# Performance work log

Hardware: AMD Instinct MI355X
Metric: run time of the kernel (lower is better)

Reference implementation:

```python
import jax, jax.numpy as jnp
import numpy as np

TOP_K = 30
NUM_RBF = 16
MAX_REL = 32  # max_relative_feature
LN_EPS = 1e-5


def normalize(x, axis=-1, eps=1e-12):
    n = jnp.linalg.norm(x, axis=axis, keepdims=True)
    return x / jnp.maximum(n, eps)


def gather_nodes(nodes, idx):
    # nodes [B,L,C], idx [B,L,K] -> [B,L,K,C]
    B, L, K = idx.shape
    flat = idx.reshape(B, L * K)
    g = jnp.take_along_axis(nodes, flat[:, :, None], axis=1)
    return g.reshape(B, L, K, -1)


def gather_edges(edges, idx):
    # edges [B,L,L,C], idx [B,L,K] -> [B,L,K,C]
    return jnp.take_along_axis(edges, idx[..., None], axis=2)


def _dist(Xca, mask, eps=1e-6):
    mask_2D = mask[:, None, :] * mask[:, :, None]            # [B,L,L]
    dX = Xca[:, None, :, :] - Xca[:, :, None, :]             # [B,L,L,3]
    D = mask_2D * jnp.sqrt(jnp.sum(dX ** 2, -1) + eps)
    D_max = jnp.max(D, -1, keepdims=True)
    D_adjust = D + (1.0 - mask_2D) * D_max
    k = min(TOP_K, Xca.shape[1])
    neg_vals, E_idx = jax.lax.top_k(-D_adjust, k)            # smallest-k
    D_neighbors = -neg_vals
    mask_neighbors = gather_edges(mask_2D[..., None], E_idx)
    return D_neighbors, E_idx, mask_neighbors


def _rbf(D):
    D_mu = jnp.linspace(2.0, 22.0, NUM_RBF)                  # [R]
    D_sigma = (22.0 - 2.0) / NUM_RBF
    return jnp.exp(-(((D[..., None] - D_mu) / D_sigma) ** 2))


def _quaternions(R):
    # R [...,3,3] -> Q [...,4]
    diag = jnp.diagonal(R, axis1=-2, axis2=-1)               # [...,3]
    Rxx, Ryy, Rzz = diag[..., 0], diag[..., 1], diag[..., 2]
    mags = 0.5 * jnp.sqrt(jnp.abs(1 + jnp.stack(
        [Rxx - Ryy - Rzz, -Rxx + Ryy - Rzz, -Rxx - Ryy + Rzz], -1)))
    signs = jnp.sign(jnp.stack([
        R[..., 2, 1] - R[..., 1, 2],
        R[..., 0, 2] - R[..., 2, 0],
        R[..., 1, 0] - R[..., 0, 1]], -1))
    xyz = signs * mags
    w = jnp.sqrt(jax.nn.relu(1 + jnp.sum(diag, -1, keepdims=True))) / 2.0
    return normalize(jnp.concatenate([xyz, w], -1))


def _get_orientations(A, B, C, E_idx, eps=1e-6):
    v1 = A - B
    v2 = C - B
    e1 = v1 / (jnp.linalg.norm(v1, axis=-1, keepdims=True) + eps)
    u2 = v2 - jnp.sum(e1 * v2, -1, keepdims=True) * e1
    e2 = u2 / (jnp.linalg.norm(u2, axis=-1, keepdims=True) + eps)
    e3 = jnp.cross(e1, e2)
    O = jnp.stack([e1, e2, e3], axis=-1)                     # [B,L,3,3] columns
    O9 = O.reshape(O.shape[0], O.shape[1], 9)
    O_nb = gather_nodes(O9, E_idx).reshape(*E_idx.shape, 3, 3)  # [B,L,K,3,3]
    B_nb = gather_nodes(B, E_idx)                            # [B,L,K,3]
    dX = B_nb - B[:, :, None, :]
    dU = normalize(jnp.einsum('blij,blkj->blki', O, dX))
    R = jnp.einsum('blji,blkjm->blkim', O, O_nb)             # O^T @ O_nb
    Q = _quaternions(R)
    return jnp.concatenate([dU, Q], -1)                      # [B,L,K,7]


def _AD_features(Xca, eps=1e-6):
    dX = Xca[:, 1:, :] - Xca[:, :-1, :]
    U = normalize(dX)
    u_2, u_1, u_0 = U[:, :-2], U[:, 1:-1], U[:, 2:]
    n_2 = normalize(jnp.cross(u_2, u_1))
    n_1 = normalize(jnp.cross(u_1, u_0))
    cosA = jnp.clip(-jnp.sum(u_1 * u_0, -1), -1 + eps, 1 - eps)
    A = jnp.arccos(cosA)
    cosD = jnp.clip(jnp.sum(n_2 * n_1, -1), -1 + eps, 1 - eps)
    D = jnp.sign(jnp.sum(u_2 * n_1, -1)) * jnp.arccos(cosD)
    AD = jnp.stack([jnp.cos(A), jnp.sin(A) * jnp.cos(D), jnp.sin(A) * jnp.sin(D)], 2)
    return jnp.pad(AD, ((0, 0), (1, 2), (0, 0)))             # [B,L,3]


def layer_norm(x, g, b):
    mu = jnp.mean(x, -1, keepdims=True)
    var = jnp.var(x, -1, keepdims=True)
    return (x - mu) / jnp.sqrt(var + LN_EPS) * g + b


def setup_inputs() -> dict:
    key = jax.random.key(0)
    ks = jax.random.split(key, 12)
    B, L = 4, 2048
    node_f, edge_f = 128, 128
    edge_in = 16 + NUM_RBF + 7 + 16  # 55 ('coarse')
    s = lambda fan: 1.0 / np.sqrt(fan)
    return {
        'X': jax.random.normal(ks[0], (B, L, 4, 3), jnp.float32),
        'mask': jnp.ones((B, L), jnp.float32),
        'residue_idx': jnp.arange(B * L, dtype=jnp.int32).reshape(B, L),
        'chain_labels': jax.random.randint(ks[1], (B, L), 0, 2, jnp.int32),
        'W_pe': jax.random.uniform(ks[2], (2 * MAX_REL + 1, 16), jnp.float32, -s(65), s(65)),
        'b_pe': jnp.zeros((16,), jnp.float32),
        'W_ch': jax.random.uniform(ks[3], (2, 16), jnp.float32, -s(2), s(2)),
        'b_ch': jnp.zeros((16,), jnp.float32),
        'W_node': jax.random.uniform(ks[4], (3, node_f), jnp.float32, -s(3), s(3)),
        'b_node': jnp.zeros((node_f,), jnp.float32),
        'W_edge': jax.random.uniform(ks[5], (edge_in, edge_f), jnp.float32, -s(edge_in), s(edge_in)),
        'b_edge': jnp.zeros((edge_f,), jnp.float32),
        'g_nodes': jnp.ones((node_f,), jnp.float32),
        'bn_nodes': jnp.zeros((node_f,), jnp.float32),
        'g_edges': jnp.ones((edge_f,), jnp.float32),
        'bn_edges': jnp.zeros((edge_f,), jnp.float32),
    }


def reference(X, mask, residue_idx, chain_labels, W_pe, b_pe, W_ch, b_ch,
              W_node, b_node, W_edge, b_edge, g_nodes, bn_nodes, g_edges, bn_edges):
    N, Ca, C = X[:, :, 0], X[:, :, 1], X[:, :, 2]
    D_neighbors, E_idx, mask_neighbors = _dist(Ca, mask)
    RBF = _rbf(D_neighbors)                                  # [B,L,K,16]
    O_features = _get_orientations(N, Ca, C, E_idx)          # [B,L,K,7]
    # positional encodings from residue-index offsets
    res_nb = jnp.take_along_axis(residue_idx[:, :, None].repeat(E_idx.shape[2], 2) * 0 +
                                 gather_nodes(residue_idx[..., None], E_idx)[..., 0], E_idx * 0, axis=2)
    res_nb = gather_nodes(residue_idx[..., None], E_idx)[..., 0]
    offset = res_nb - residue_idx[:, :, None]
    d = jnp.clip(offset + MAX_REL, 0, 2 * MAX_REL)
    E_positional = W_pe[d] + b_pe                            # [B,L,K,16]
    # chain embedding from same/other-chain indicator
    ch_nb = gather_nodes(chain_labels[..., None], E_idx)[..., 0]
    same = (ch_nb == chain_labels[:, :, None]).astype(jnp.float32)
    E_chains = jnp.stack([same, 1.0 - same], -1) @ W_ch + b_ch  # [B,L,K,16]
    E = jnp.concatenate([E_positional, RBF, O_features, E_chains], -1)
    E = layer_norm(E @ W_edge + b_edge, g_edges, bn_edges)
    V = _AD_features(Ca)                                     # [B,L,3]
    V = layer_norm(V @ W_node + b_node, g_nodes, bn_nodes)
    return V, E, E_idx
```

## Files before the change

kernel.cpp:

```cpp
#include <hip/hip_runtime.h>

#define NB 4
#define NL 2048
#define NK 30
#define NRES (NB*NL)
#define NEDGE (NRES*NK)
#define EPB 16

enum : int {
  WOFF_DNB   = 0,
  WOFF_EIDX  = 245760,
  WOFF_O     = 491520,
  WOFF_WPE   = 565248,
  WOFF_BPE   = 566288,
  WOFF_WCH   = 566304,
  WOFF_BCH   = 566336,
  WOFF_WNODE = 566352,
  WOFF_BNODE = 566736,
  WOFF_WEDGE = 566864,
  WOFF_BEDGE = 573904,
  WOFF_GN    = 574032,
  WOFF_BNN   = 574160,
  WOFF_GE    = 574288,
  WOFF_BNE   = 574416,
  WOFF_PK    = 574544,
};

__device__ __forceinline__ float sgnf(float x) {
  return (x > 0.f) ? 1.f : ((x < 0.f) ? -1.f : 0.f);
}
__device__ __forceinline__ float loadf(const void* p, int idx, bool isbf) {
  if (isbf) return __uint_as_float(((unsigned)((const unsigned short*)p)[idx]) << 16);
  return ((const float*)p)[idx];
}
__device__ __forceinline__ int geti(const void* p, int idx, int mode) {
  if (mode == 0) return ((const int*)p)[idx];
  if (mode == 1) return (int)rintf(((const float*)p)[idx]);
  return (int)rintf(__uint_as_float(((unsigned)((const unsigned short*)p)[idx]) << 16));
}
__device__ __forceinline__ bool probe_bf(const void* maskp) {
  return ((const unsigned*)maskp)[0] == 0x3F803F80u;
}
__device__ __forceinline__ int probe_int(const void* residxp) {
  unsigned w1 = ((const unsigned*)residxp)[1];
  return (w1 == 1u) ? 0 : ((w1 == 0x3F800000u) ? 1 : 2);
}
__device__ __forceinline__ unsigned long long shfl_xor_u64(unsigned long long x, int m) {
  int lo = (int)(unsigned)(x & 0xffffffffull);
  int hi = (int)(unsigned)(x >> 32);
  lo = __shfl_xor(lo, m, 64);
  hi = __shfl_xor(hi, m, 64);
  return ((unsigned long long)(unsigned)hi << 32) | (unsigned)lo;
}

struct ConvArgs {
  const void* src[12];
  int off[12];
  int sz[12];
  const void* maskp;
};

__global__ void prep_kernel(ConvArgs a, float* wsf) {
  const bool isbf = probe_bf(a.maskp);
  const int stride = gridDim.x * blockDim.x;
  const int t0 = blockIdx.x * blockDim.x + threadIdx.x;
  for (int q = 0; q < 12; ++q) {
    float* dst = wsf + a.off[q];
    const int n = a.sz[q];
    for (int i = t0; i < n; i += stride) dst[i] = loadf(a.src[q], i, isbf);
  }
}

__global__ void frames_kernel(const void* Xraw, const void* maskp, float* wsf) {
  const bool isbf = probe_bf(maskp);
  int r = blockIdx.x * blockDim.x + threadIdx.x;
  if (r >= NRES) return;
  const int xb = r * 12;
  float nx = loadf(Xraw, xb+0, isbf), ny = loadf(Xraw, xb+1, isbf), nz = loadf(Xraw, xb+2, isbf);
  float cax= loadf(Xraw, xb+3, isbf), cay= loadf(Xraw, xb+4, isbf), caz= loadf(Xraw, xb+5, isbf);
  float cx = loadf(Xraw, xb+6, isbf), cy = loadf(Xraw, xb+7, isbf), cz = loadf(Xraw, xb+8, isbf);
  float mk = loadf(maskp, r, isbf);
  float4* pko = (float4*)(wsf + WOFF_PK);
  pko[r] = make_float4(cax, cay, caz, mk);
  float v1x=nx-cax, v1y=ny-cay, v1z=nz-caz;
  float v2x=cx-cax, v2y=cy-cay, v2z=cz-caz;
  float n1 = sqrtf(v1x*v1x + v1y*v1y + v1z*v1z) + 1e-6f;
  float e1x=v1x/n1, e1y=v1y/n1, e1z=v1z/n1;
  float dp = e1x*v2x + e1y*v2y + e1z*v2z;
  float u2x=v2x-dp*e1x, u2y=v2y-dp*e1y, u2z=v2z-dp*e1z;
  float n2 = sqrtf(u2x*u2x + u2y*u2y + u2z*u2z) + 1e-6f;
  float e2x=u2x/n2, e2y=u2y/n2, e2z=u2z/n2;
  float e3x = e1y*e2z - e1z*e2y;
  float e3y = e1z*e2x - e1x*e2z;
  float e3z = e1x*e2y - e1y*e2x;
  float* o = wsf + WOFF_O + (size_t)r*9;
  o[0]=e1x; o[1]=e2x; o[2]=e3x;
  o[3]=e1y; o[4]=e2y; o[5]=e3y;
  o[6]=e1z; o[7]=e2z; o[8]=e3z;
}

#define CE(i,j) { unsigned long long a_=q[i], b_=q[j]; bool lt_=a_<b_; \
                  q[i]=lt_?a_:b_; q[j]=lt_?b_:a_; }
#define SORT8(B) CE(B+0,B+1) CE(B+2,B+3) CE(B+4,B+5) CE(B+6,B+7) \
                 CE(B+0,B+2) CE(B+1,B+3) CE(B+4,B+6) CE(B+5,B+7) \
                 CE(B+1,B+2) CE(B+5,B+6) \
                 CE(B+0,B+4) CE(B+1,B+5) CE(B+2,B+6) CE(B+3,B+7) \
                 CE(B+2,B+4) CE(B+3,B+5) \
                 CE(B+1,B+2) CE(B+3,B+4) CE(B+5,B+6)
#define SHIFTQ(B) { q[B+0]=q[B+1]; q[B+1]=q[B+2]; q[B+2]=q[B+3]; q[B+3]=q[B+4]; \
                    q[B+4]=q[B+5]; q[B+5]=q[B+6]; q[B+6]=q[B+7]; q[B+7]=~0ull; }

__global__ __launch_bounds__(256) void topk_kernel(const float* wsf,
                                                   int* eidx, float* dnb,
                                                   float* outf, unsigned long long outEidx) {
#pragma clang fp contract(off)
  const int lane = threadIdx.x & 63;
  const int row = blockIdx.x*4 + (threadIdx.x >> 6);
  const int b = row >> 11, i = row & (NL-1);
  const float4* pb = ((const float4*)(wsf + WOFF_PK)) + b*NL;
  const float4 pi = pb[i];
  const float xi = pi.x, yi = pi.y, zi = pi.z, mi = pi.w;
  unsigned long long q[32];
  float lmax = -1e30f;
  #pragma unroll
  for (int s=0;s<32;s++){
    float4 pj = pb[s*64 + lane];
    float dx=pj.x-xi, dy=pj.y-yi, dz=pj.z-zi;
    float ss = dx*dx;
    ss = ss + dy*dy;
    ss = ss + dz*dz;
    ss = ss + 1e-6f;
    float m2 = mi*pj.w;
    float d = m2 * sqrtf(ss);
    lmax = fmaxf(lmax, d);
    q[s] = ((unsigned long long)__float_as_uint(d) << 32) | (unsigned)(s*64 + lane);
  }
  #pragma unroll
  for (int m=1;m<64;m<<=1) lmax = fmaxf(lmax, __shfl_xor(lmax, m, 64));
  const unsigned dmb = __float_as_uint(lmax);
  #pragma unroll
  for (int s=0;s<32;s++)
    if ((unsigned)(q[s] >> 32) == 0u)
      q[s] = ((unsigned long long)dmb << 32) | (unsigned)q[s];
  SORT8(0) SORT8(8) SORT8(16) SORT8(24)
  const size_t obase = (size_t)row*NK;
  #pragma unroll 1
  for (int k=0;k<NK;k++){
    unsigned long long c01 = q[0]  < q[8]  ? q[0]  : q[8];
    unsigned long long c23 = q[16] < q[24] ? q[16] : q[24];
    unsigned long long cand = c01 < c23 ? c01 : c23;
    unsigned long long best = cand;
    #pragma unroll
    for (int m=1;m<64;m<<=1){
      unsigned long long o2 = shfl_xor_u64(best, m);
      best = o2 < best ? o2 : best;
    }
    if (lane==0){
      unsigned j = (unsigned)best;
      eidx[obase + k] = (int)j;
      dnb[obase + k] = __uint_as_float((unsigned)(best >> 32));
      outf[outEidx + obase + k] = (float)j;
    }
    if (cand == best){
      if      (q[0]  == best) SHIFTQ(0)
      else if (q[8]  == best) SHIFTQ(8)
      else if (q[16] == best) SHIFTQ(16)
      else                    SHIFTQ(24)
    }
  }
}

__global__ __launch_bounds__(256) void edge_kernel(const float* wsf, const int* eidx,
                                                   const void* Xraw, const void* maskp,
                                                   const void* residx, const void* chains,
                                                   float* outf, unsigned long long outE) {
  __shared__ float WL[55*128];
  __shared__ float F[55][EPB];
  const bool isbf = probe_bf(maskp);
  const int icmode = probe_int(residx);
  const int t = threadIdx.x;
  {
    const float2* Wg = (const float2*)(wsf + WOFF_WEDGE);
    float2* Wl = (float2*)WL;
    #pragma unroll
    for (int k = 0; k < 14; ++k) {
      int idx = t + k*256;
      if (idx < 55*64) Wl[idx] = Wg[idx];
    }
  }
  const int g = t & 15, s = t >> 4;
  const int e = blockIdx.x * EPB + g;
  const int row = e / NK;
  const int b = row / NL, i = row % NL;
  const int j = eidx[e];
  {
    int ri = geti(residx, b*NL + i, icmode), rj = geti(residx, b*NL + j, icmode);
    int d = rj - ri + 32;
    d = d < 0 ? 0 : (d > 64 ? 64 : d);
    F[s][g] = wsf[WOFF_WPE + d*16 + s] + wsf[WOFF_BPE + s];
  }
  {
    float D = wsf[WOFF_DNB + e];
    float mu = (float)(2.0 + s * (20.0 / 15.0));
    float tt = (D - mu) / 1.25f;
    F[16+s][g] = expf(-(tt*tt));
  }
  {
    int ci = geti(chains, b*NL + i, icmode), cj = geti(chains, b*NL + j, icmode);
    float w = (ci == cj) ? wsf[WOFF_WCH + s] : wsf[WOFF_WCH + 16 + s];
    F[39+s][g] = w + wsf[WOFF_BCH + s];
  }
  if (s == 0) {
    const float* Oi = wsf + WOFF_O + (size_t)row*9;
    const float* Oj = wsf + WOFF_O + ((size_t)(b*NL + j))*9;
    const int ci_ = row*12 + 3, cj_ = (b*NL + j)*12 + 3;
    float dx = loadf(Xraw, cj_+0, isbf) - loadf(Xraw, ci_+0, isbf);
    float dy = loadf(Xraw, cj_+1, isbf) - loadf(Xraw, ci_+1, isbf);
    float dz = loadf(Xraw, cj_+2, isbf) - loadf(Xraw, ci_+2, isbf);
    float du0 = Oi[0]*dx + Oi[1]*dy + Oi[2]*dz;
    float du1 = Oi[3]*dx + Oi[4]*dy + Oi[5]*dz;
    float du2 = Oi[6]*dx + Oi[7]*dy + Oi[8]*dz;
    float n = fmaxf(sqrtf(du0*du0 + du1*du1 + du2*du2), 1e-12f);
    F[32][g] = du0/n; F[33][g] = du1/n; F[34][g] = du2/n;
    float R[3][3];
    #pragma unroll
    for (int a2=0;a2<3;a2++)
      #pragma unroll
      for (int m=0;m<3;m++)
        R[a2][m] = Oi[0*3+a2]*Oj[0*3+m] + Oi[1*3+a2]*Oj[1*3+m] + Oi[2*3+a2]*Oj[2*3+m];
    float mx = 0.5f*sqrtf(fabsf(1.0f + R[0][0] - R[1][1] - R[2][2]));
    float my = 0.5f*sqrtf(fabsf(1.0f - R[0][0] + R[1][1] - R[2][2]));
    float mz = 0.5f*sqrtf(fabsf(1.0f - R[0][0] - R[1][1] + R[2][2]));
    float qx = sgnf(R[2][1]-R[1][2]) * mx;
    float qy = sgnf(R[0][2]-R[2][0]) * my;
    float qz = sgnf(R[1][0]-R[0][1]) * mz;
    float qw = sqrtf(fmaxf(1.0f + R[0][0] + R[1][1] + R[2][2], 0.0f)) / 2.0f;
    float qn = fmaxf(sqrtf(qx*qx + qy*qy + qz*qz + qw*qw), 1e-12f);
    F[35][g] = qx/qn; F[36][g] = qy/qn; F[37][g] = qz/qn; F[38][g] = qw/qn;
  }
  __syncthreads();
  const int wv = t >> 6, lane = t & 63;
  const int ge = wv*4;
  const int c0 = 2*lane;
  const float be0 = wsf[WOFF_BEDGE + c0], be1 = wsf[WOFF_BEDGE + c0 + 1];
  float acc[4][2];
  #pragma unroll
  for (int qq=0;qq<4;qq++){ acc[qq][0]=be0; acc[qq][1]=be1; }
  for (int d = 0; d < 55; ++d) {
    float2 w2 = *((const float2*)&WL[d*128 + c0]);
    float4 f4 = *((const float4*)&F[d][ge]);
    acc[0][0] = fmaf(f4.x, w2.x, acc[0][0]); acc[0][1] = fmaf(f4.x, w2.y, acc[0][1]);
    acc[1][0] = fmaf(f4.y, w2.x, acc[1][0]); acc[1][1] = fmaf(f4.y, w2.y, acc[1][1]);
    acc[2][0] = fmaf(f4.z, w2.x, acc[2][0]); acc[2][1] = fmaf(f4.z, w2.y, acc[2][1]);
    acc[3][0] = fmaf(f4.w, w2.x, acc[3][0]); acc[3][1] = fmaf(f4.w, w2.y, acc[3][1]);
  }
  const float ge0 = wsf[WOFF_GE + c0], ge1 = wsf[WOFF_GE + c0 + 1];
  const float bn0 = wsf[WOFF_BNE + c0], bn1 = wsf[WOFF_BNE + c0 + 1];
  #pragma unroll
  for (int qq=0;qq<4;qq++){
    float sum = acc[qq][0] + acc[qq][1];
    for (int m=1;m<64;m<<=1) sum += __shfl_xor(sum, m, 64);
    float mu_ = sum * (1.0f/128.0f);
    float d0 = acc[qq][0] - mu_, d1 = acc[qq][1] - mu_;
    float v = d0*d0 + d1*d1;
    for (int m=1;m<64;m<<=1) v += __shfl_xor(v, m, 64);
    float inv = 1.0f / sqrtf(v * (1.0f/128.0f) + 1e-5f);
    float2 pk;
    pk.x = d0*inv*ge0 + bn0;
    pk.y = d1*inv*ge1 + bn1;
    *((float2*)(outf + outE + (size_t)(blockIdx.x*EPB + ge + qq)*128 + c0)) = pk;
  }
}

__global__ __launch_bounds__(256) void node_kernel(const float* wsf, const void* Xraw,
                                                   const void* maskp, float* outf) {
  const bool isbf = probe_bf(maskp);
  const int gw = (blockIdx.x * 256 + threadIdx.x) >> 6;
  const int lane = threadIdx.x & 63;
  const int b = gw / NL, l = gw % NL;
  float ad0 = 0.f, ad1 = 0.f, ad2 = 0.f;
  if (l >= 1 && l <= NL - 3) {
    const int base = (b*NL)*12;
    float p0x = loadf(Xraw, base+(l-1)*12+3, isbf), p0y = loadf(Xraw, base+(l-1)*12+4, isbf), p0z = loadf(Xraw, base+(l-1)*12+5, isbf);
    float p1x = loadf(Xraw, base+(l  )*12+3, isbf), p1y = loadf(Xraw, base+(l  )*12+4, isbf), p1z = loadf(Xraw, base+(l  )*12+5, isbf);
    float p2x = loadf(Xraw, base+(l+1)*12+3, isbf), p2y = loadf(Xraw, base+(l+1)*12+4, isbf), p2z = loadf(Xraw, base+(l+1)*12+5, isbf);
    float p3x = loadf(Xraw, base+(l+2)*12+3, isbf), p3y = loadf(Xraw, base+(l+2)*12+4, isbf), p3z = loadf(Xraw, base+(l+2)*12+5, isbf);
    float u2x=p1x-p0x, u2y=p1y-p0y, u2z=p1z-p0z;
    float u1x=p2x-p1x, u1y=p2y-p1y, u1z=p2z-p1z;
    float u0x=p3x-p2x, u0y=p3y-p2y, u0z=p3z-p2z;
    float nn;
    nn = fmaxf(sqrtf(u2x*u2x+u2y*u2y+u2z*u2z), 1e-12f); u2x/=nn; u2y/=nn; u2z/=nn;
    nn = fmaxf(sqrtf(u1x*u1x+u1y*u1y+u1z*u1z), 1e-12f); u1x/=nn; u1y/=nn; u1z/=nn;
    nn = fmaxf(sqrtf(u0x*u0x+u0y*u0y+u0z*u0z), 1e-12f); u0x/=nn; u0y/=nn; u0z/=nn;
    float n2x = u2y*u1z - u2z*u1y, n2y = u2z*u1x - u2x*u1z, n2z = u2x*u1y - u2y*u1x;
    float n1x = u1y*u0z - u1z*u0y, n1y = u1z*u0x - u1x*u0z, n1z = u1x*u0y - u1y*u0x;
    nn = fmaxf(sqrtf(n2x*n2x+n2y*n2y+n2z*n2z), 1e-12f); n2x/=nn; n2y/=nn; n2z/=nn;
    nn = fmaxf(sqrtf(n1x*n1x+n1y*n1y+n1z*n1z), 1e-12f); n1x/=nn; n1y/=nn; n1z/=nn;
    const float lo = (float)(-1.0 + 1e-6), hi = (float)(1.0 - 1e-6);
    float cosA = -(u1x*u0x + u1y*u0y + u1z*u0z);
    cosA = fminf(fmaxf(cosA, lo), hi);
    float A = acosf(cosA);
    float cosD = n2x*n1x + n2y*n1y + n2z*n1z;
    cosD = fminf(fmaxf(cosD, lo), hi);
    float Dd = sgnf(u2x*n1x + u2y*n1y + u2z*n1z) * acosf(cosD);
    ad0 = cosf(A);
    ad1 = sinf(A) * cosf(Dd);
    ad2 = sinf(A) * sinf(Dd);
  }
  const int c0 = 2*lane, c1 = c0 + 1;
  float acc0 = wsf[WOFF_BNODE+c0] + ad0*wsf[WOFF_WNODE+c0] + ad1*wsf[WOFF_WNODE+128+c0] + ad2*wsf[WOFF_WNODE+256+c0];
  float acc1 = wsf[WOFF_BNODE+c1] + ad0*wsf[WOFF_WNODE+c1] + ad1*wsf[WOFF_WNODE+128+c1] + ad2*wsf[WOFF_WNODE+256+c1];
  float s = acc0 + acc1;
  for (int m=1;m<64;m<<=1) s += __shfl_xor(s, m, 64);
  float mu_ = s * (1.0f/128.0f);
  float d0 = acc0 - mu_, d1 = acc1 - mu_;
  float v = d0*d0 + d1*d1;
  for (int m=1;m<64;m<<=1) v += __shfl_xor(v, m, 64);
  float inv = 1.0f / sqrtf(v * (1.0f/128.0f) + 1e-5f);
  float y0 = d0*inv*wsf[WOFF_GN + c0] + wsf[WOFF_BNN + c0];
  float y1 = d1*inv*wsf[WOFF_GN + c1] + wsf[WOFF_BNN + c1];
  float2 pk; pk.x = y0; pk.y = y1;
  *((float2*)(outf + (size_t)gw*128 + c0)) = pk;
}

extern "C" void kernel_launch(void* const* d_in, const int* in_sizes, int n_in,
                              void* d_out, int out_size, void* d_ws, size_t ws_size,
                              hipStream_t stream) {
  float* wsf = (float*)d_ws;
  int* eidx = (int*)(wsf + WOFF_EIDX);
  float* dnb = wsf + WOFF_DNB;
  float* outf = (float*)d_out;
  const void* Xraw = d_in[0];
  const void* maskp = d_in[1];

  unsigned long long outEidx = (unsigned long long)out_size - NEDGE;
  unsigned long long outE    = outEidx - (unsigned long long)NEDGE*128;

  ConvArgs ca;
  const int fsz[12]  = {1040, 16, 32, 16, 384, 128, 7040, 128, 128, 128, 128, 128};
  const int foff[12] = {WOFF_WPE, WOFF_BPE, WOFF_WCH, WOFF_BCH, WOFF_WNODE, WOFF_BNODE,
                        WOFF_WEDGE, WOFF_BEDGE, WOFF_GN, WOFF_BNN, WOFF_GE, WOFF_BNE};
  for (int q = 0; q < 12; ++q) { ca.src[q] = d_in[4 + q]; ca.off[q] = foff[q]; ca.sz[q] = fsz[q]; }
  ca.maskp = maskp;

  prep_kernel<<<40, 256, 0, stream>>>(ca, wsf);
  frames_kernel<<<NRES/256, 256, 0, stream>>>(Xraw, maskp, wsf);
  topk_kernel<<<NRES/4, 256, 0, stream>>>(wsf, eidx, dnb, outf, outEidx);
  edge_kernel<<<NEDGE/EPB, 256, 0, stream>>>(wsf, eidx, Xraw, maskp, d_in[2], d_in[3], outf, outE);
  node_kernel<<<NRES/4, 256, 0, stream>>>(wsf, Xraw, maskp, outf);
}
```

Baseline: 338.3 us.

## Process 64 edges per block and speed up top-k wave argmin

The edge kernel now handles 64 edges per block instead of 16. Each thread computes four feature channels, and each wave accumulates 16 edges, so every shared-memory weight load is reused across more edges, and the weight copy into shared memory uses float4 loads. The top-k selection now runs a float min reduction followed by a ballot, and falls back to the 64-bit shuffle reduction only when distances tie, which halves the shuffle traffic in the common case. The costs are more registers for the accumulators, a block count cut to a quarter, and the extra ballot logic.

```diff
diff --git a/kernel.cpp b/kernel.cpp
--- a/kernel.cpp
+++ b/kernel.cpp
@@ -5,7 +5,7 @@
 #define NK 30
 #define NRES (NB*NL)
 #define NEDGE (NRES*NK)
-#define EPB 16
+#define EPB 64
 
 enum : int {
   WOFF_DNB   = 0,
@@ -149,11 +149,23 @@
     unsigned long long c01 = q[0]  < q[8]  ? q[0]  : q[8];
     unsigned long long c23 = q[16] < q[24] ? q[16] : q[24];
     unsigned long long cand = c01 < c23 ? c01 : c23;
-    unsigned long long best = cand;
+    float dh = __uint_as_float((unsigned)(cand >> 32));
+    float dmin = dh;
     #pragma unroll
-    for (int m=1;m<64;m<<=1){
-      unsigned long long o2 = shfl_xor_u64(best, m);
-      best = o2 < best ? o2 : best;
+    for (int m=1;m<64;m<<=1) dmin = fminf(dmin, __shfl_xor(dmin, m, 64));
+    unsigned long long bal = __ballot(dh == dmin);
+    unsigned long long best;
+    if (__popcll(bal) == 1) {
+      int src = __ffsll((long long)bal) - 1;
+      int lo = __shfl((int)(unsigned)cand, src, 64);
+      best = ((unsigned long long)__float_as_uint(dmin) << 32) | (unsigned)lo;
+    } else {
+      best = cand;
+      #pragma unroll
+      for (int m=1;m<64;m<<=1){
+        unsigned long long o2 = shfl_xor_u64(best, m);
+        best = o2 < best ? o2 : best;
+      }
     }
     if (lane==0){
       unsigned j = (unsigned)best;
@@ -180,37 +192,35 @@
   const int icmode = probe_int(residx);
   const int t = threadIdx.x;
   {
-    const float2* Wg = (const float2*)(wsf + WOFF_WEDGE);
-    float2* Wl = (float2*)WL;
+    const float4* Wg = (const float4*)(wsf + WOFF_WEDGE);
+    float4* Wl = (float4*)WL;
     #pragma unroll
-    for (int k = 0; k < 14; ++k) {
+    for (int k = 0; k < 7; ++k) {
       int idx = t + k*256;
-      if (idx < 55*64) Wl[idx] = Wg[idx];
+      if (idx < 55*32) Wl[idx] = Wg[idx];
     }
   }
-  const int g = t & 15, s = t >> 4;
+  const int g = t & 63, sq = t >> 6;
   const int e = blockIdx.x * EPB + g;
   const int row = e / NK;
   const int b = row / NL, i = row % NL;
   const int j = eidx[e];
-  {
-    int ri = geti(residx, b*NL + i, icmode), rj = geti(residx, b*NL + j, icmode);
-    int d = rj - ri + 32;
-    d = d < 0 ? 0 : (d > 64 ? 64 : d);
-    F[s][g] = wsf[WOFF_WPE + d*16 + s] + wsf[WOFF_BPE + s];
-  }
-  {
-    float D = wsf[WOFF_DNB + e];
+  const int ri = geti(residx, b*NL + i, icmode), rj = geti(residx, b*NL + j, icmode);
+  int dd = rj - ri + 32;
+  dd = dd < 0 ? 0 : (dd > 64 ? 64 : dd);
+  const int ci = geti(chains, b*NL + i, icmode), cj = geti(chains, b*NL + j, icmode);
+  const float D = wsf[WOFF_DNB + e];
+  #pragma unroll
+  for (int u = 0; u < 4; ++u) {
+    const int s = sq*4 + u;
+    F[s][g] = wsf[WOFF_WPE + dd*16 + s] + wsf[WOFF_BPE + s];
     float mu = (float)(2.0 + s * (20.0 / 15.0));
     float tt = (D - mu) / 1.25f;
     F[16+s][g] = expf(-(tt*tt));
-  }
-  {
-    int ci = geti(chains, b*NL + i, icmode), cj = geti(chains, b*NL + j, icmode);
     float w = (ci == cj) ? wsf[WOFF_WCH + s] : wsf[WOFF_WCH + 16 + s];
     F[39+s][g] = w + wsf[WOFF_BCH + s];
   }
-  if (s == 0) {
+  if (sq == 0) {
     const float* Oi = wsf + WOFF_O + (size_t)row*9;
     const float* Oj = wsf + WOFF_O + ((size_t)(b*NL + j))*9;
     const int ci_ = row*12 + 3, cj_ = (b*NL + j)*12 + 3;
@@ -240,24 +250,37 @@
   }
   __syncthreads();
   const int wv = t >> 6, lane = t & 63;
-  const int ge = wv*4;
+  const int ge = wv*16;
   const int c0 = 2*lane;
   const float be0 = wsf[WOFF_BEDGE + c0], be1 = wsf[WOFF_BEDGE + c0 + 1];
-  float acc[4][2];
-  #pragma unroll
-  for (int qq=0;qq<4;qq++){ acc[qq][0]=be0; acc[qq][1]=be1; }
+  float acc[16][2];
+  #pragma unroll
+  for (int qq=0;qq<16;qq++){ acc[qq][0]=be0; acc[qq][1]=be1; }
   for (int d = 0; d < 55; ++d) {
     float2 w2 = *((const float2*)&WL[d*128 + c0]);
-    float4 f4 = *((const float4*)&F[d][ge]);
-    acc[0][0] = fmaf(f4.x, w2.x, acc[0][0]); acc[0][1] = fmaf(f4.x, w2.y, acc[0][1]);
-    acc[1][0] = fmaf(f4.y, w2.x, acc[1][0]); acc[1][1] = fmaf(f4.y, w2.y, acc[1][1]);
-    acc[2][0] = fmaf(f4.z, w2.x, acc[2][0]); acc[2][1] = fmaf(f4.z, w2.y, acc[2][1]);
-    acc[3][0] = fmaf(f4.w, w2.x, acc[3][0]); acc[3][1] = fmaf(f4.w, w2.y, acc[3][1]);
+    const float4* Fd = (const float4*)&F[d][ge];
+    float4 fa = Fd[0], fb = Fd[1], fc = Fd[2], fd4 = Fd[3];
+    acc[0][0]  = fmaf(fa.x,  w2.x, acc[0][0]);  acc[0][1]  = fmaf(fa.x,  w2.y, acc[0][1]);
+    acc[1][0]  = fmaf(fa.y,  w2.x, acc[1][0]);  acc[1][1]  = fmaf(fa.y,  w2.y, acc[1][1]);
+    acc[2][0]  = fmaf(fa.z,  w2.x, acc[2][0]);  acc[2][1]  = fmaf(fa.z,  w2.y, acc[2][1]);
+    acc[3][0]  = fmaf(fa.w,  w2.x, acc[3][0]);  acc[3][1]  = fmaf(fa.w,  w2.y, acc[3][1]);
+    acc[4][0]  = fmaf(fb.x,  w2.x, acc[4][0]);  acc[4][1]  = fmaf(fb.x,  w2.y, acc[4][1]);
+    acc[5][0]  = fmaf(fb.y,  w2.x, acc[5][0]);  acc[5][1]  = fmaf(fb.y,  w2.y, acc[5][1]);
+    acc[6][0]  = fmaf(fb.z,  w2.x, acc[6][0]);  acc[6][1]  = fmaf(fb.z,  w2.y, acc[6][1]);
+    acc[7][0]  = fmaf(fb.w,  w2.x, acc[7][0]);  acc[7][1]  = fmaf(fb.w,  w2.y, acc[7][1]);
+    acc[8][0]  = fmaf(fc.x,  w2.x, acc[8][0]);  acc[8][1]  = fmaf(fc.x,  w2.y, acc[8][1]);
+    acc[9][0]  = fmaf(fc.y,  w2.x, acc[9][0]);  acc[9][1]  = fmaf(fc.y,  w2.y, acc[9][1]);
+    acc[10][0] = fmaf(fc.z,  w2.x, acc[10][0]); acc[10][1] = fmaf(fc.z,  w2.y, acc[10][1]);
+    acc[11][0] = fmaf(fc.w,  w2.x, acc[11][0]); acc[11][1] = fmaf(fc.w,  w2.y, acc[11][1]);
+    acc[12][0] = fmaf(fd4.x, w2.x, acc[12][0]); acc[12][1] = fmaf(fd4.x, w2.y, acc[12][1]);
+    acc[13][0] = fmaf(fd4.y, w2.x, acc[13][0]); acc[13][1] = fmaf(fd4.y, w2.y, acc[13][1]);
+    acc[14][0] = fmaf(fd4.z, w2.x, acc[14][0]); acc[14][1] = fmaf(fd4.z, w2.y, acc[14][1]);
+    acc[15][0] = fmaf(fd4.w, w2.x, acc[15][0]); acc[15][1] = fmaf(fd4.w, w2.y, acc[15][1]);
   }
   const float ge0 = wsf[WOFF_GE + c0], ge1 = wsf[WOFF_GE + c0 + 1];
   const float bn0 = wsf[WOFF_BNE + c0], bn1 = wsf[WOFF_BNE + c0 + 1];
   #pragma unroll
-  for (int qq=0;qq<4;qq++){
+  for (int qq=0;qq<16;qq++){
     float sum = acc[qq][0] + acc[qq][1];
     for (int m=1;m<64;m<<=1) sum += __shfl_xor(sum, m, 64);
     float mu_ = sum * (1.0f/128.0f);
```

Result: faster. 318.2 us (-5.9%).
